# Kernel optimization log

Measured on AMD Instinct MI355X. Metric: run time of the kernel, lower is better.

Reference implementation:

```python
import jax, jax.numpy as jnp
import numpy as np
from jax import lax

EPS = 1e-5


def _dcn_core(value, offset, mask, offset_scale):
    # value: (B,H,W,G,D); offset: (B,H,W,G,K,2) as (dx,dy); mask: (B,H,W,G,K)
    # DCNv4: no softmax on mask; sampling loc = center + (kernel_grid + offset)*offset_scale
    B, H, W, G, D = value.shape
    K = mask.shape[-1]
    P = H * W
    kr = jnp.arange(3, dtype=value.dtype) - 1.0
    gy, gx = jnp.meshgrid(kr, kr, indexing="ij")  # 3x3 kernel grid
    gx = gx.reshape(1, 1, 1, 1, K)
    gy = gy.reshape(1, 1, 1, 1, K)
    bx = jnp.arange(W, dtype=value.dtype).reshape(1, 1, W, 1, 1)
    by = jnp.arange(H, dtype=value.dtype).reshape(1, H, 1, 1, 1)
    ix = bx + (gx + offset[..., 0]) * offset_scale  # (B,H,W,G,K) pixel-index coords
    iy = by + (gy + offset[..., 1]) * offset_scale

    tog = lambda a: a.transpose(0, 3, 1, 2, 4).reshape(B, G, P, K)
    ix, iy, m = tog(ix), tog(iy), tog(mask)
    vflat = value.transpose(0, 3, 1, 2, 4).reshape(B, G, P, D)

    x0 = jnp.floor(ix)
    y0 = jnp.floor(iy)
    tx = ix - x0
    ty = iy - y0
    out = jnp.zeros((B, G, P, D), value.dtype)
    # bilinear with zero padding (grid_sample padding_mode='zeros', align_corners=False)
    for dy, dx, wgt in ((0, 0, (1 - ty) * (1 - tx)), (0, 1, (1 - ty) * tx),
                        (1, 0, ty * (1 - tx)), (1, 1, ty * tx)):
        xc = x0 + dx
        yc = y0 + dy
        valid = ((xc >= 0) & (xc < W) & (yc >= 0) & (yc < H)).astype(value.dtype)
        lin = (jnp.clip(yc, 0, H - 1) * W + jnp.clip(xc, 0, W - 1)).astype(jnp.int32)
        v = jnp.take_along_axis(vflat, lin.reshape(B, G, P * K, 1), axis=2)
        v = v.reshape(B, G, P, K, D)
        out = out + jnp.einsum("bgpk,bgpkd->bgpd", wgt * m * valid, v)
    return out.transpose(0, 2, 1, 3).reshape(B, P, G * D)


def setup_inputs() -> dict:
    key = jax.random.key(0)
    ks = jax.random.split(key, 6)
    C = 64
    r = lambda k, shp, s: jax.random.normal(k, shp, jnp.float32) * s
    return {
        "x": r(ks[0], (8, C, 128, 128), 1.0),
        "vp_w": r(ks[1], (C, C), C ** -0.5),
        "vp_b": jnp.zeros((C,), jnp.float32),
        "dw_w": r(ks[2], (C, 1, 3, 3), 1.0 / 3.0),
        "dw_b": jnp.zeros((C,), jnp.float32),
        "om_w": r(ks[3], (56, C), 0.01),
        "om_b": jnp.zeros((56,), jnp.float32),
        "op_w": r(ks[4], (C, C), C ** -0.5),
        "op_b": jnp.zeros((C,), jnp.float32),
        "bn_g": jnp.ones((C // 2,), jnp.float32),
        "bn_b": jnp.zeros((C // 2,), jnp.float32),
        "bn_m": jnp.zeros((C // 2,), jnp.float32),
        "bn_v": jnp.ones((C // 2,), jnp.float32),
    }


def reference(x, vp_w, vp_b, dw_w, dw_b, om_w, om_b, op_w, op_b, bn_g, bn_b, bn_m, bn_v):
    B, C, H, W = x.shape
    G, K, OS = 2, 9, 2.0  # group = in_planes//out_planes = 2; 3x3 -> K=9
    seq = x.reshape(B, H * W, C)  # raw reshape exactly as the torch code
    # DCNv4 value_proj
    val = seq @ vp_w.T + vp_b
    value = val.reshape(B, H, W, G, C // G)
    # offset/mask branch: depthwise 3x3 conv on raw input, then linear
    xi = seq.reshape(B, H, W, C).transpose(0, 3, 1, 2)  # (B,C,H,W)
    dw = lax.conv_general_dilated(xi, dw_w, (1, 1), "SAME",
                                  dimension_numbers=("NCHW", "OIHW", "NCHW"),
                                  feature_group_count=C)
    dw = dw + dw_b[None, :, None, None]
    om = dw.transpose(0, 2, 3, 1) @ om_w.T + om_b  # (B,H,W,56)
    om = om[..., : G * K * 3].reshape(B, H, W, G, 3 * K)  # drop pad-to-8 tail
    offset = om[..., : 2 * K].reshape(B, H, W, G, K, 2)
    mask = om[..., 2 * K:]
    core = _dcn_core(value, offset, mask, OS)  # (B, HW, C)
    out = (core @ op_w.T + op_b).reshape(B, C, H, W)  # raw reshape, as in torch code
    z = 0.5 * (out[:, : C // 2] + out[:, C // 2:])  # chunk + average
    z = bn_g[:, None, None] * (z - bn_m[:, None, None]) * lax.rsqrt(bn_v + EPS)[:, None, None] + bn_b[:, None, None]
    return jnp.maximum(z, 0.0)
```

## Files before the change

kernel.cpp:

```cpp
#include <hip/hip_runtime.h>

#define B_ 8
#define H_ 128
#define W_ 128
#define P_ 16384
#define C_ 64
#define NQ (B_*P_)

static __device__ __forceinline__ void fma4s(float4& a, float s, const float4& v) {
  a.x += s * v.x; a.y += s * v.y; a.z += s * v.z; a.w += s * v.w;
}
static __device__ __forceinline__ void fma4e(float4& a, const float4& u, const float4& v) {
  a.x += u.x * v.x; a.y += u.y * v.y; a.z += u.z * v.z; a.w += u.w * v.w;
}

__global__ __launch_bounds__(256) void gemm64_kernel(
    const float* __restrict__ X, const float* __restrict__ W,
    const float* __restrict__ bias, float* __restrict__ Y) {
  __shared__ __align__(16) float Ws[64][68];
  __shared__ __align__(16) float XsT[64][68];
  int tid = threadIdx.x;
  size_t row0 = (size_t)blockIdx.x * 64;
#pragma unroll
  for (int i0 = 0; i0 < 4096; i0 += 1024) {
    int i = i0 + tid * 4;
    int a = i >> 6, k = i & 63;
    float4 wv = *(const float4*)(W + i);
    Ws[k][a] = wv.x; Ws[k + 1][a] = wv.y; Ws[k + 2][a] = wv.z; Ws[k + 3][a] = wv.w;
    float4 xv = *(const float4*)(X + row0 * 64 + i);
    XsT[k][a] = xv.x; XsT[k + 1][a] = xv.y; XsT[k + 2][a] = xv.z; XsT[k + 3][a] = xv.w;
  }
  __syncthreads();
  int ty = tid >> 4, tx = tid & 15;
  int r0 = ty * 4, c0 = tx * 4;
  float4 b4 = *(const float4*)(bias + c0);
  float4 acc0 = b4, acc1 = b4, acc2 = b4, acc3 = b4;
#pragma unroll 8
  for (int k = 0; k < 64; ++k) {
    float4 wv = *(const float4*)&Ws[k][c0];
    float4 xv = *(const float4*)&XsT[k][r0];
    fma4s(acc0, xv.x, wv);
    fma4s(acc1, xv.y, wv);
    fma4s(acc2, xv.z, wv);
    fma4s(acc3, xv.w, wv);
  }
  float* yb = Y + (row0 + r0) * 64 + c0;
  *(float4*)(yb) = acc0;
  *(float4*)(yb + 64) = acc1;
  *(float4*)(yb + 128) = acc2;
  *(float4*)(yb + 192) = acc3;
}

__global__ __launch_bounds__(256) void dwom_kernel(
    const float* __restrict__ X, const float* __restrict__ dw_w,
    const float* __restrict__ dw_b, const float* __restrict__ om_w,
    const float* __restrict__ om_b, float* __restrict__ OM) {
  __shared__ __align__(16) float dwsT[64][68];
  __shared__ __align__(16) float omwT[64][60];
  __shared__ __align__(16) float dwwT[9][68];
  __shared__ __align__(16) float dwbs[64];
  __shared__ __align__(16) float ombs[56];
  int tid = threadIdx.x;
  for (int i = tid; i < 3456; i += 256) omwT[i & 63][i >> 6] = om_w[i];
  for (int i = tid; i < 576; i += 256) dwwT[i % 9][i / 9] = dw_w[i];
  if (tid < 64) dwbs[tid] = dw_b[tid];
  if (tid < 56) ombs[tid] = (tid < 54) ? om_b[tid] : 0.f;
  int q0 = blockIdx.x * 64;
  int b = q0 >> 14;
  int p0 = q0 & 16383;
  int h = p0 >> 7, w0 = p0 & 127;
  __syncthreads();

  {
    int cv = tid & 15;
    int lqq = tid >> 4;
    int c0 = cv * 4;
    const float* xb = X + (size_t)b * 1048576;
    float4 wt[9];
#pragma unroll
    for (int t = 0; t < 9; ++t) wt[t] = *(const float4*)&dwwT[t][c0];
    float4 dwb4 = *(const float4*)&dwbs[c0];
#pragma unroll
    for (int it = 0; it < 4; ++it) {
      int lq = lqq + 16 * it;
      int ww = w0 + lq;
      float4 acc = dwb4;
#pragma unroll
      for (int t = 0; t < 9; ++t) {
        int dy = t / 3 - 1, dx = t % 3 - 1;
        int hh = h + dy, wx = ww + dx;
        if ((unsigned)hh < 128u && (unsigned)wx < 128u) {
          float4 v = *(const float4*)(xb + (((size_t)(hh * 128 + wx)) << 6) + c0);
          fma4e(acc, v, wt[t]);
        }
      }
      dwsT[c0][lq] = acc.x; dwsT[c0 + 1][lq] = acc.y;
      dwsT[c0 + 2][lq] = acc.z; dwsT[c0 + 3][lq] = acc.w;
    }
  }
  __syncthreads();

  int ty = tid >> 4, tx = tid & 15;
  int r0 = ty * 4, o0 = tx * 4;
  if (o0 < 54) {
    float4 b4 = *(const float4*)&ombs[o0];
    float4 acc0 = b4, acc1 = b4, acc2 = b4, acc3 = b4;
#pragma unroll 8
    for (int k = 0; k < 64; ++k) {
      float4 ov = *(const float4*)&omwT[k][o0];
      float4 dv = *(const float4*)&dwsT[k][r0];
      fma4s(acc0, dv.x, ov);
      fma4s(acc1, dv.y, ov);
      fma4s(acc2, dv.z, ov);
      fma4s(acc3, dv.w, ov);
    }
    float accs[4][4] = {{acc0.x, acc0.y, acc0.z, acc0.w},
                        {acc1.x, acc1.y, acc1.z, acc1.w},
                        {acc2.x, acc2.y, acc2.z, acc2.w},
                        {acc3.x, acc3.y, acc3.z, acc3.w}};
#pragma unroll
    for (int i2 = 0; i2 < 4; i2++) {
      size_t base = (size_t)(q0 + r0 + i2) * 54 + o0;
#pragma unroll
      for (int j = 0; j < 4; j++)
        if (o0 + j < 54) OM[base + j] = accs[i2][j];
    }
  }
}

__global__ __launch_bounds__(256) void dcn_kernel(
    const float* __restrict__ val, const float* __restrict__ OM,
    float* __restrict__ core) {
  __shared__ __align__(16) float oms[16 * 54];
  int tid = threadIdx.x;
  int q0 = blockIdx.x * 16;
  if (tid < 216)
    ((float4*)oms)[tid] = ((const float4*)(OM + (size_t)q0 * 54))[tid];
  __syncthreads();
  int lq = tid >> 4;
  int g = (tid >> 3) & 1;
  int dv = tid & 7;
  int q = q0 + lq;
  int b = q >> 14;
  int p = q & 16383;
  int h = p >> 7, w = p & 127;
  const float* og = oms + lq * 54 + g * 27;
  const float* vbase = val + (size_t)b * 1048576 + g * 32 + dv * 4;
  float fw = (float)w, fh = (float)h;
  float4 acc = make_float4(0.f, 0.f, 0.f, 0.f);
#pragma unroll
  for (int k = 0; k < 9; ++k) {
    float offx = og[2 * k], offy = og[2 * k + 1], m = og[18 + k];
    float ix = fw + ((float)(k % 3) - 1.0f + offx) * 2.0f;
    float iy = fh + ((float)(k / 3) - 1.0f + offy) * 2.0f;
    float x0f = floorf(ix), y0f = floorf(iy);
    float tx = ix - x0f, ty = iy - y0f;
    int x0 = (int)x0f, y0 = (int)y0f;
    int x1 = x0 + 1, y1 = y0 + 1;
    float w00 = (1.f - ty) * (1.f - tx) * m;
    float w01 = (1.f - ty) * tx * m;
    float w10 = ty * (1.f - tx) * m;
    float w11 = ty * tx * m;
    bool vx0 = (unsigned)x0 < 128u, vx1 = (unsigned)x1 < 128u;
    bool vy0 = (unsigned)y0 < 128u, vy1 = (unsigned)y1 < 128u;
    if (vy0 && vx0) fma4s(acc, w00, *(const float4*)(vbase + (size_t)((y0 * 128 + x0) << 6)));
    if (vy0 && vx1) fma4s(acc, w01, *(const float4*)(vbase + (size_t)((y0 * 128 + x1) << 6)));
    if (vy1 && vx0) fma4s(acc, w10, *(const float4*)(vbase + (size_t)((y1 * 128 + x0) << 6)));
    if (vy1 && vx1) fma4s(acc, w11, *(const float4*)(vbase + (size_t)((y1 * 128 + x1) << 6)));
  }
  ((float4*)core)[(size_t)q * 16 + g * 8 + dv] = acc;
}

__global__ __launch_bounds__(256) void final_kernel(
    const float* __restrict__ proj, const float* __restrict__ bn_g,
    const float* __restrict__ bn_b, const float* __restrict__ bn_m,
    const float* __restrict__ bn_v, float* __restrict__ out) {
  int i = (blockIdx.x * 256 + threadIdx.x) * 4;
  int c2 = (i >> 14) & 31;
  int b = i >> 19;
  size_t f1 = (size_t)i + (size_t)b * 524288;
  float4 a = *(const float4*)(proj + f1);
  float4 c = *(const float4*)(proj + f1 + 524288);
  float scale = bn_g[c2] * rsqrtf(bn_v[c2] + 1e-5f);
  float shift = bn_b[c2] - bn_m[c2] * scale;
  float4 z;
  z.x = fmaxf(0.5f * (a.x + c.x) * scale + shift, 0.f);
  z.y = fmaxf(0.5f * (a.y + c.y) * scale + shift, 0.f);
  z.z = fmaxf(0.5f * (a.z + c.z) * scale + shift, 0.f);
  z.w = fmaxf(0.5f * (a.w + c.w) * scale + shift, 0.f);
  *(float4*)(out + i) = z;
}

extern "C" void kernel_launch(void* const* d_in, const int* in_sizes, int n_in,
                              void* d_out, int out_size, void* d_ws, size_t ws_size,
                              hipStream_t stream) {
  const float* x    = (const float*)d_in[0];
  const float* vp_w = (const float*)d_in[1];
  const float* vp_b = (const float*)d_in[2];
  const float* dw_w = (const float*)d_in[3];
  const float* dw_b = (const float*)d_in[4];
  const float* om_w = (const float*)d_in[5];
  const float* om_b = (const float*)d_in[6];
  const float* op_w = (const float*)d_in[7];
  const float* op_b = (const float*)d_in[8];
  const float* bn_g = (const float*)d_in[9];
  const float* bn_b = (const float*)d_in[10];
  const float* bn_m = (const float*)d_in[11];
  const float* bn_v = (const float*)d_in[12];

  float* ws   = (float*)d_ws;
  float* val  = ws;
  float* core = ws + 8388608;
  float* om   = ws + 16777216;
  float* proj = ws;

  gemm64_kernel<<<dim3(NQ / 64), dim3(256), 0, stream>>>(x, vp_w, vp_b, val);
  dwom_kernel<<<dim3(NQ / 64), dim3(256), 0, stream>>>(x, dw_w, dw_b, om_w, om_b, om);
  dcn_kernel<<<dim3(NQ / 16), dim3(256), 0, stream>>>(val, om, core);
  gemm64_kernel<<<dim3(NQ / 64), dim3(256), 0, stream>>>(core, op_w, op_b, proj);
  final_kernel<<<dim3(out_size / 1024), dim3(256), 0, stream>>>(proj, bn_g, bn_b, bn_m, bn_v, (float*)d_out);
}
```

Before: 150.1 us.

## Fuse deformable sampling, output projection, and batchnorm-ReLU epilogue into one kernel

Merges the DCN sampling kernel, the output-projection GEMM and the chunk-average/BN/ReLU kernel into a single kernel. Each block samples 32 pixels (two rows spaced half an image apart, matching the raw-reshape chunk pairing), keeps the core tile in shared memory, projects it with op_w staged in shared memory, and writes the final activated output directly. This removes the core and proj round trips through global memory and two launches. Bilinear gathers become branchless by clamping indices and zeroing weights, which adds loads for out-of-bounds corners. Each block also reloads the 64x64 weight matrix.

```diff
diff --git a/kernel.cpp b/kernel.cpp
--- a/kernel.cpp
+++ b/kernel.cpp
@@ -128,67 +128,104 @@
   }
 }
 
-__global__ __launch_bounds__(256) void dcn_kernel(
+__global__ __launch_bounds__(256) void dcn_fused_kernel(
     const float* __restrict__ val, const float* __restrict__ OM,
-    float* __restrict__ core) {
-  __shared__ __align__(16) float oms[16 * 54];
+    const float* __restrict__ op_w, const float* __restrict__ op_b,
+    const float* __restrict__ bn_g, const float* __restrict__ bn_b,
+    const float* __restrict__ bn_m, const float* __restrict__ bn_v,
+    float* __restrict__ out) {
+  __shared__ __align__(16) float oms[32 * 54];
+  __shared__ __align__(16) float cs[32][68];
+  __shared__ __align__(16) float Ws[64][68];
   int tid = threadIdx.x;
-  int q0 = blockIdx.x * 16;
-  if (tid < 216)
-    ((float4*)oms)[tid] = ((const float4*)(OM + (size_t)q0 * 54))[tid];
-  __syncthreads();
-  int lq = tid >> 4;
-  int g = (tid >> 3) & 1;
-  int dv = tid & 7;
-  int q = q0 + lq;
-  int b = q >> 14;
-  int p = q & 16383;
-  int h = p >> 7, w = p & 127;
-  const float* og = oms + lq * 54 + g * 27;
-  const float* vbase = val + (size_t)b * 1048576 + g * 32 + dv * 4;
-  float fw = (float)w, fh = (float)h;
-  float4 acc = make_float4(0.f, 0.f, 0.f, 0.f);
-#pragma unroll
-  for (int k = 0; k < 9; ++k) {
-    float offx = og[2 * k], offy = og[2 * k + 1], m = og[18 + k];
-    float ix = fw + ((float)(k % 3) - 1.0f + offx) * 2.0f;
-    float iy = fh + ((float)(k / 3) - 1.0f + offy) * 2.0f;
-    float x0f = floorf(ix), y0f = floorf(iy);
-    float tx = ix - x0f, ty = iy - y0f;
-    int x0 = (int)x0f, y0 = (int)y0f;
-    int x1 = x0 + 1, y1 = y0 + 1;
-    float w00 = (1.f - ty) * (1.f - tx) * m;
-    float w01 = (1.f - ty) * tx * m;
-    float w10 = ty * (1.f - tx) * m;
-    float w11 = ty * tx * m;
-    bool vx0 = (unsigned)x0 < 128u, vx1 = (unsigned)x1 < 128u;
-    bool vy0 = (unsigned)y0 < 128u, vy1 = (unsigned)y1 < 128u;
-    if (vy0 && vx0) fma4s(acc, w00, *(const float4*)(vbase + (size_t)((y0 * 128 + x0) << 6)));
-    if (vy0 && vx1) fma4s(acc, w01, *(const float4*)(vbase + (size_t)((y0 * 128 + x1) << 6)));
-    if (vy1 && vx0) fma4s(acc, w10, *(const float4*)(vbase + (size_t)((y1 * 128 + x0) << 6)));
-    if (vy1 && vx1) fma4s(acc, w11, *(const float4*)(vbase + (size_t)((y1 * 128 + x1) << 6)));
-  }
-  ((float4*)core)[(size_t)q * 16 + g * 8 + dv] = acc;
-}
-
-__global__ __launch_bounds__(256) void final_kernel(
-    const float* __restrict__ proj, const float* __restrict__ bn_g,
-    const float* __restrict__ bn_b, const float* __restrict__ bn_m,
-    const float* __restrict__ bn_v, float* __restrict__ out) {
-  int i = (blockIdx.x * 256 + threadIdx.x) * 4;
-  int c2 = (i >> 14) & 31;
-  int b = i >> 19;
-  size_t f1 = (size_t)i + (size_t)b * 524288;
-  float4 a = *(const float4*)(proj + f1);
-  float4 c = *(const float4*)(proj + f1 + 524288);
+  int bid = blockIdx.x;
+  int b = bid >> 9;
+  int p0 = (bid & 511) * 16;
+  int q0lo = b * 16384 + p0;
+
+#pragma unroll
+  for (int i0 = 0; i0 < 4096; i0 += 1024) {
+    int i = i0 + tid * 4;
+    int c = i >> 6, k = i & 63;
+    float4 wv = *(const float4*)(op_w + i);
+    Ws[k][c] = wv.x; Ws[k + 1][c] = wv.y; Ws[k + 2][c] = wv.z; Ws[k + 3][c] = wv.w;
+  }
+  if (tid < 216) {
+    ((float4*)oms)[tid] = ((const float4*)(OM + (size_t)q0lo * 54))[tid];
+    ((float4*)(oms + 864))[tid] = ((const float4*)(OM + (size_t)(q0lo + 8192) * 54))[tid];
+  }
+  __syncthreads();
+
+  {
+    int lq = tid >> 4;
+    int g = (tid >> 3) & 1;
+    int dv = tid & 7;
+    const float* vbase = val + (size_t)b * 1048576 + g * 32 + dv * 4;
+#pragma unroll
+    for (int t = 0; t < 2; ++t) {
+      int row = t * 16 + lq;
+      int p = p0 + t * 8192 + lq;
+      int h = p >> 7, w = p & 127;
+      const float* og = oms + row * 54 + g * 27;
+      float fw = (float)w, fh = (float)h;
+      float4 acc = make_float4(0.f, 0.f, 0.f, 0.f);
+#pragma unroll
+      for (int k = 0; k < 9; ++k) {
+        float offx = og[2 * k], offy = og[2 * k + 1], m = og[18 + k];
+        float ix = fw + ((float)(k % 3) - 1.0f + offx) * 2.0f;
+        float iy = fh + ((float)(k / 3) - 1.0f + offy) * 2.0f;
+        float x0f = floorf(ix), y0f = floorf(iy);
+        float tx = ix - x0f, ty = iy - y0f;
+        int x0 = (int)x0f, y0 = (int)y0f;
+        int x1 = x0 + 1, y1 = y0 + 1;
+        float vx0 = ((unsigned)x0 < 128u) ? 1.f : 0.f;
+        float vx1 = ((unsigned)x1 < 128u) ? 1.f : 0.f;
+        float vy0 = ((unsigned)y0 < 128u) ? 1.f : 0.f;
+        float vy1 = ((unsigned)y1 < 128u) ? 1.f : 0.f;
+        int xc0 = min(max(x0, 0), 127), xc1 = min(max(x1, 0), 127);
+        int yc0 = min(max(y0, 0), 127), yc1 = min(max(y1, 0), 127);
+        float w00 = (1.f - ty) * (1.f - tx) * m * vy0 * vx0;
+        float w01 = (1.f - ty) * tx * m * vy0 * vx1;
+        float w10 = ty * (1.f - tx) * m * vy1 * vx0;
+        float w11 = ty * tx * m * vy1 * vx1;
+        fma4s(acc, w00, *(const float4*)(vbase + (size_t)((yc0 * 128 + xc0) << 6)));
+        fma4s(acc, w01, *(const float4*)(vbase + (size_t)((yc0 * 128 + xc1) << 6)));
+        fma4s(acc, w10, *(const float4*)(vbase + (size_t)((yc1 * 128 + xc0) << 6)));
+        fma4s(acc, w11, *(const float4*)(vbase + (size_t)((yc1 * 128 + xc1) << 6)));
+      }
+      *(float4*)&cs[row][g * 32 + dv * 4] = acc;
+    }
+  }
+  __syncthreads();
+
+  int ty = tid >> 4, tx = tid & 15;
+  int c0 = tx * 4;
+  float4 bias4 = *(const float4*)(op_b + c0);
+  float4 accA = bias4, accB = bias4;
+#pragma unroll 4
+  for (int k0 = 0; k0 < 64; k0 += 4) {
+    float4 a4 = *(const float4*)&cs[ty][k0];
+    float4 b4 = *(const float4*)&cs[ty + 16][k0];
+    float4 w0 = *(const float4*)&Ws[k0][c0];
+    float4 w1 = *(const float4*)&Ws[k0 + 1][c0];
+    float4 w2 = *(const float4*)&Ws[k0 + 2][c0];
+    float4 w3 = *(const float4*)&Ws[k0 + 3][c0];
+    fma4s(accA, a4.x, w0); fma4s(accA, a4.y, w1);
+    fma4s(accA, a4.z, w2); fma4s(accA, a4.w, w3);
+    fma4s(accB, b4.x, w0); fma4s(accB, b4.y, w1);
+    fma4s(accB, b4.z, w2); fma4s(accB, b4.w, w3);
+  }
+
+  int f = (p0 + ty) * 64 + c0;
+  int c2 = f >> 14;
   float scale = bn_g[c2] * rsqrtf(bn_v[c2] + 1e-5f);
   float shift = bn_b[c2] - bn_m[c2] * scale;
   float4 z;
-  z.x = fmaxf(0.5f * (a.x + c.x) * scale + shift, 0.f);
-  z.y = fmaxf(0.5f * (a.y + c.y) * scale + shift, 0.f);
-  z.z = fmaxf(0.5f * (a.z + c.z) * scale + shift, 0.f);
-  z.w = fmaxf(0.5f * (a.w + c.w) * scale + shift, 0.f);
-  *(float4*)(out + i) = z;
+  z.x = fmaxf(0.5f * (accA.x + accB.x) * scale + shift, 0.f);
+  z.y = fmaxf(0.5f * (accA.y + accB.y) * scale + shift, 0.f);
+  z.z = fmaxf(0.5f * (accA.z + accB.z) * scale + shift, 0.f);
+  z.w = fmaxf(0.5f * (accA.w + accB.w) * scale + shift, 0.f);
+  *(float4*)(out + (size_t)b * 524288 + f) = z;
 }
 
 extern "C" void kernel_launch(void* const* d_in, const int* in_sizes, int n_in,
@@ -210,13 +247,10 @@
 
   float* ws   = (float*)d_ws;
   float* val  = ws;
-  float* core = ws + 8388608;
   float* om   = ws + 16777216;
-  float* proj = ws;
 
   gemm64_kernel<<<dim3(NQ / 64), dim3(256), 0, stream>>>(x, vp_w, vp_b, val);
   dwom_kernel<<<dim3(NQ / 64), dim3(256), 0, stream>>>(x, dw_w, dw_b, om_w, om_b, om);
-  dcn_kernel<<<dim3(NQ / 16), dim3(256), 0, stream>>>(val, om, core);
-  gemm64_kernel<<<dim3(NQ / 64), dim3(256), 0, stream>>>(core, op_w, op_b, proj);
-  final_kernel<<<dim3(out_size / 1024), dim3(256), 0, stream>>>(proj, bn_g, bn_b, bn_m, bn_v, (float*)d_out);
-}
+  dcn_fused_kernel<<<dim3(4096), dim3(256), 0, stream>>>(
+      val, om, op_w, op_b, bn_g, bn_b, bn_m, bn_v, (float*)d_out);
+}
```

Result: faster. 132.7 us (-11.6%).
